# Kernel tuning notes

Hardware: AMD Instinct MI355X
Metric: run time of the kernel (lower is better)

The kernel has to match this reference:

```python
import jax, jax.numpy as jnp
import numpy as np

S = 15      # subject_nums
C = 2048    # in_channels (extractor output dim)
NC = 3      # num_classes
B = 1024    # subject_batch_num (rows per subject)
SUBJ = 7    # target subject
KERNEL_MUL = 2.0
KERNEL_NUM = 5


def setup_inputs() -> dict:
    key = jax.random.key(0)
    k = jax.random.split(key, 5)
    x = jax.random.normal(k[0], (S * B, C), dtype=jnp.float32)
    labels = jax.random.randint(k[1], (S * B,), 0, NC)
    y = jax.nn.one_hot(labels, NC, dtype=jnp.float32)
    subject_label = jnp.repeat(jnp.arange(S, dtype=jnp.int32), B)
    W_add = 0.02 * jax.random.normal(k[2], (S, 512, C), dtype=jnp.float32)
    b_add = jnp.zeros((S, 512), dtype=jnp.float32)
    W_cls = 0.02 * jax.random.normal(k[3], (S, NC, 512), dtype=jnp.float32)
    b_cls = jnp.zeros((S, NC), dtype=jnp.float32)
    return {"x": x, "y": y, "subject_label": subject_label,
            "W_add": W_add, "b_add": b_add, "W_cls": W_cls, "b_cls": b_cls,
            "subject": SUBJ}


def _mmd(source, target):
    # Standard multi-kernel Gaussian MMD (DAN-style), as used in the repo.
    n = source.shape[0]
    total = jnp.concatenate([source, target], axis=0)      # [2n, d]
    sq = jnp.sum(total * total, axis=-1)
    d2 = sq[:, None] + sq[None, :] - 2.0 * (total @ total.T)  # [2n, 2n]
    m = 2 * n
    bandwidth = jnp.sum(d2) / (m * m - m)
    bandwidth = bandwidth / (KERNEL_MUL ** (KERNEL_NUM // 2))
    kernels = sum(jnp.exp(-d2 / (bandwidth * (KERNEL_MUL ** i))) for i in range(KERNEL_NUM))
    XX = kernels[:n, :n]
    YY = kernels[n:, n:]
    XY = kernels[:n, n:]
    YX = kernels[n:, :n]
    return jnp.mean(XX + YY - XY - YX)


def reference(x, y, subject_label, W_add, b_add, W_cls, b_cls, subject):
    S_ = W_add.shape[0]
    b = x.shape[0] // S_          # == (subject_label == subject).sum() by construction
    K = S_ - 1
    idx = np.array([i for i in range(S_) if i != subject])  # static: subject is a Python int

    xr = x.reshape(S_, b, -1)
    src = xr[idx]                 # [K, b, C] source-subject blocks
    tgt = xr[subject]             # [b, C] target-subject block
    Wk, bk = W_add[idx], b_add[idx]

    # Grouped per-subject addblock Linear(C -> 512)
    outs = jnp.einsum('kbc,kdc->kbd', src, Wk) + bk[:, None, :]       # [K, b, 512]
    t_outs = jnp.einsum('bc,kdc->kbd', tgt, Wk) + bk[:, None, :]      # [K, b, 512]

    # Class predictors: ReLU + Linear(512 -> NC), predictors 0..K-1 are used
    Wc, bc = W_cls[:K], b_cls[:K]
    logits = jnp.einsum('kbd,knd->kbn', jax.nn.relu(outs), Wc) + bc[:, None, :]
    t_logits = jnp.einsum('kbd,knd->kbn', jax.nn.relu(t_outs), Wc) + bc[:, None, :]

    # ---- MMD loss ----
    mmd_loss = jnp.mean(jax.vmap(_mmd)(outs, t_outs))

    # ---- DISC loss: pairwise |softmax - softmax| over source features ----
    P = jax.nn.softmax(outs, axis=-1)                                  # [K, b, 512]
    disc_loss = 0.0
    for i in range(K - 1):  # fixed small loop over subjects, inner term vectorized
        disc_loss = disc_loss + jnp.abs(P[i + 1:] - P[i]).mean(axis=(1, 2)).sum()
    disc_loss = disc_loss * 2.0 / (K * (K - 1))

    # ---- CLS loss: KL(one-hot/soft target || log_softmax(logits)) ----
    yr = y.reshape(S_, b, -1)[idx]                                     # [K, b, NC]
    logp = jax.nn.log_softmax(logits, axis=-1)
    safe_y = jnp.where(yr > 0, yr, 1.0)
    kl = jnp.where(yr > 0, yr * (jnp.log(safe_y) - logp), 0.0)         # 0*log0 -> 0 (torch kl_div)
    cls_loss = kl.sum(-1).mean()

    # ---- PRED ACC on target subject ----
    t_prob = jax.nn.softmax(t_logits, axis=-1).mean(axis=0)            # [b, NC]
    y_tgt = y.reshape(S_, b, -1)[subject]
    pred = jnp.sum(jnp.argmax(t_prob, axis=1) == jnp.argmax(y_tgt, axis=1))
    nums = b

    return (mmd_loss * 0.1, disc_loss * 0.4, cls_loss, pred, nums)
```

## Files before the change

kernel.cpp:

```cpp
#include <hip/hip_runtime.h>
#include <hip/hip_bf16.h>
#include <stdint.h>

typedef __attribute__((ext_vector_type(8))) __bf16 bf16x8;
typedef __attribute__((ext_vector_type(4))) float f32x4;

#define CDIM 2048
#define DDIM 512

__device__ __forceinline__ unsigned short f2bf(float f) {
  union { float f; unsigned u; } a; a.f = f;
  unsigned r = a.u + 0x7FFFu + ((a.u >> 16) & 1u);
  return (unsigned short)(r >> 16);
}
__device__ __forceinline__ float bf2f(unsigned short h) {
  union { unsigned u; float f; } a; a.u = ((unsigned)h) << 16;
  return a.f;
}

typedef const __attribute__((address_space(1))) void gas_void;
typedef __attribute__((address_space(3))) void las_void;
__device__ __forceinline__ void async16(const void* g, void* l) {
  __builtin_amdgcn_global_load_lds((gas_void*)g, (las_void*)l, 16, 0, 0);
}

#define VMW(n) asm volatile("s_waitcnt vmcnt(" #n ")" ::: "memory")
#define SBAR() __builtin_amdgcn_s_barrier()
#define SFENCE() __builtin_amdgcn_sched_barrier(0)

__device__ __forceinline__ float blockSum256(float v) {
  __shared__ float sh[4];
  #pragma unroll
  for (int o = 32; o; o >>= 1) v += __shfl_xor(v, o, 64);
  int lane = threadIdx.x & 63, w = threadIdx.x >> 6;
  __syncthreads();
  if (lane == 0) sh[w] = v;
  __syncthreads();
  return sh[0] + sh[1] + sh[2] + sh[3];
}

__device__ __forceinline__ bf16x8 lds_frag(const unsigned short* base, int row, int cb) {
  return *(const bf16x8*)(base + row*64 + (((cb ^ (row & 7))) << 3));
}

__global__ __launch_bounds__(256) void k_convert(const float* __restrict__ x,
    const float* __restrict__ w, uint2* __restrict__ x16, uint2* __restrict__ w16) {
  const int nx4 = 15*1024*CDIM/4;
  const int nw4 = 15*DDIM*CDIM/4;
  int stride = gridDim.x * blockDim.x;
  for (int i = blockIdx.x*blockDim.x + threadIdx.x; i < nx4; i += stride) {
    float4 v = ((const float4*)x)[i];
    x16[i] = make_uint2((unsigned)f2bf(v.x) | ((unsigned)f2bf(v.y) << 16),
                        (unsigned)f2bf(v.z) | ((unsigned)f2bf(v.w) << 16));
  }
  for (int i = blockIdx.x*blockDim.x + threadIdx.x; i < nw4; i += stride) {
    float4 v = ((const float4*)w)[i];
    w16[i] = make_uint2((unsigned)f2bf(v.x) | ((unsigned)f2bf(v.y) << 16),
                        (unsigned)f2bf(v.z) | ((unsigned)f2bf(v.w) << 16));
  }
}

__global__ __launch_bounds__(512, 2) void k_gemm1(
    const unsigned short* __restrict__ x16,
    const unsigned short* __restrict__ w16,
    const float* __restrict__ b_add,
    const int* __restrict__ subj_p,
    unsigned short* __restrict__ t16)
{
  const int subj = *subj_p;
  int bid = blockIdx.x;
  int k  = bid >> 5;
  int t  = bid & 31;
  int mt = t >> 1, nt = t & 1;
  int ik = (k < subj) ? k : (k + 1);

  __shared__ unsigned short lds[3*384*64];

  int tid = threadIdx.x;
  int lane = tid & 63;
  int w = tid >> 6;
  int wm = w >> 2, wn = w & 3;
  int rr = lane >> 3;
  int cc8 = ((lane & 7) ^ rr) << 3;

  const unsigned short* Bb = w16 + (size_t)ik * DDIM * CDIM;

  f32x4 acc[4][4];
  #pragma unroll
  for (int a = 0; a < 4; a++)
    #pragma unroll
    for (int b = 0; b < 4; b++) acc[a][b] = f32x4{0.f,0.f,0.f,0.f};

  auto stage = [&](int tt, int bufi) {
    unsigned short* buf = lds + bufi*(384*64);
    int ks = tt*64;
    #pragma unroll
    for (int i = 0; i < 2; i++) {
      int r0 = (w*2 + i)*8;
      int gr = mt*128 + r0 + rr;
      int xrow = ((gr < 1024) ? ik : subj)*1024 + (gr & 1023);
      async16(x16 + (size_t)xrow*CDIM + ks + cc8, buf + r0*64);
    }
    #pragma unroll
    for (int i = 0; i < 4; i++) {
      int r0 = (w*4 + i)*8;
      int gn = nt*256 + r0 + rr;
      async16(Bb + (size_t)gn*CDIM + ks + cc8, buf + 8192 + r0*64);
    }
  };

  auto compute = [&](int bufi) {
    const unsigned short* A = lds + bufi*(384*64);
    const unsigned short* B = A + 8192;
    bf16x8 af[4][2], bfr[4][2];
    #pragma unroll
    for (int a = 0; a < 4; a++)
      #pragma unroll
      for (int ksl = 0; ksl < 2; ksl++)
        af[a][ksl] = lds_frag(A, wm*64 + a*16 + (lane & 15), ksl*4 + (lane >> 4));
    #pragma unroll
    for (int bb = 0; bb < 4; bb++)
      #pragma unroll
      for (int ksl = 0; ksl < 2; ksl++)
        bfr[bb][ksl] = lds_frag(B, wn*64 + bb*16 + (lane & 15), ksl*4 + (lane >> 4));
    __builtin_amdgcn_s_setprio(1);
    #pragma unroll
    for (int a = 0; a < 4; a++)
      #pragma unroll
      for (int bb = 0; bb < 4; bb++) {
        acc[a][bb] = __builtin_amdgcn_mfma_f32_16x16x32_bf16(af[a][0], bfr[bb][0], acc[a][bb], 0, 0, 0);
        acc[a][bb] = __builtin_amdgcn_mfma_f32_16x16x32_bf16(af[a][1], bfr[bb][1], acc[a][bb], 0, 0, 0);
      }
    __builtin_amdgcn_s_setprio(0);
  };

  stage(0, 0);
  stage(1, 1);
  VMW(6); SBAR(); SFENCE();

  int cur = 0;
  for (int tt = 0; tt < 30; ++tt) {
    int nb = cur + 2; if (nb >= 3) nb -= 3;
    stage(tt + 2, nb);
    compute(cur);
    VMW(6); SBAR(); SFENCE();
    cur = (cur == 2) ? 0 : cur + 1;
  }
  compute(cur);
  VMW(0); SBAR(); SFENCE();
  cur = (cur == 2) ? 0 : cur + 1;
  compute(cur);

  const float* bias = b_add + ik*DDIM;
  #pragma unroll
  for (int bb = 0; bb < 4; bb++) {
    int coln = nt*256 + wn*64 + bb*16 + (lane & 15);
    float bv = bias[coln];
    #pragma unroll
    for (int a = 0; a < 4; a++) {
      #pragma unroll
      for (int r = 0; r < 4; r++) {
        int rowm = mt*128 + wm*64 + a*16 + ((lane >> 4) << 2) + r;
        t16[((size_t)k*2048 + rowm)*DDIM + coln] = f2bf(acc[a][bb][r] + bv);
      }
    }
  }
}

__global__ __launch_bounds__(256) void k_rowred(const unsigned short* __restrict__ t16,
    float* __restrict__ sq, float* __restrict__ rmax, float* __restrict__ rinv)
{
  int wid = blockIdx.x*4 + (threadIdx.x >> 6);
  int lane = threadIdx.x & 63;
  uint4 v = *(const uint4*)(t16 + (size_t)wid * DDIM + lane*8);
  unsigned uu[4] = {v.x, v.y, v.z, v.w};
  float f[8];
  #pragma unroll
  for (int q = 0; q < 4; q++) {
    f[2*q]   = bf2f((unsigned short)(uu[q] & 0xffffu));
    f[2*q+1] = bf2f((unsigned short)(uu[q] >> 16));
  }
  float s2 = 0.f, mx = -3.4e38f;
  #pragma unroll
  for (int j = 0; j < 8; j++) { s2 += f[j]*f[j]; mx = fmaxf(mx, f[j]); }
  #pragma unroll
  for (int o = 32; o; o >>= 1) { s2 += __shfl_xor(s2, o, 64); mx = fmaxf(mx, __shfl_xor(mx, o, 64)); }
  float se = 0.f;
  #pragma unroll
  for (int j = 0; j < 8; j++) se += __expf(f[j] - mx);
  #pragma unroll
  for (int o = 32; o; o >>= 1) se += __shfl_xor(se, o, 64);
  if (lane == 0) { sq[wid] = s2; rmax[wid] = mx; rinv[wid] = 1.f/se; }
}

__global__ __launch_bounds__(256) void k_colsum(const unsigned short* __restrict__ t16,
    float* __restrict__ scol)
{
  int b = blockIdx.x;
  int k = b >> 4, sub = b & 15;
  int d = ((sub & 1) << 8) + threadIdx.x;
  int r0 = (sub >> 1) << 8;
  const unsigned short* base = t16 + (size_t)k*2048*DDIM;
  float s = 0.f;
  for (int r = r0; r < r0 + 256; r++) s += bf2f(base[(size_t)r*DDIM + d]);
  atomicAdd(&scol[k*DDIM + d], s);
}

__global__ __launch_bounds__(256) void k_bw(const float* __restrict__ sq,
    const float* __restrict__ scol, float* __restrict__ c2)
{
  int k = blockIdx.x;
  float a = 0.f;
  for (int r = threadIdx.x; r < 2048; r += 256) a += sq[k*2048 + r];
  float b = 0.f;
  for (int d = threadIdx.x; d < 512; d += 256) { float v = scol[k*512 + d]; b += v*v; }
  float atot = blockSum256(a);
  float btot = blockSum256(b);
  if (threadIdx.x == 0) {
    float sumd2 = 2.f*2048.f*atot - 2.f*btot;
    float bw = sumd2 / (2048.f*2048.f - 2048.f) * 0.25f;
    #pragma unroll
    for (int i = 0; i < 5; i++)
      c2[k*5 + i] = -1.4426950408889634f / (bw * (float)(1 << i));
  }
}

__global__ __launch_bounds__(256, 1) void k_mmd(
    const unsigned short* __restrict__ t16,
    const float* __restrict__ sq,
    const float* __restrict__ c2,
    float* __restrict__ g_acc)
{
  int bid = blockIdx.x;
  int k = bid / 136;
  int tri = bid - k*136;
  int it = 0;
  while (tri >= 16 - it) { tri -= 16 - it; it++; }
  int jt = it + tri;

  const unsigned short* T = t16 + (size_t)k * 2048 * DDIM;

  __shared__ unsigned short lds[3*256*64];
  __shared__ float sqs[256];

  int tid = threadIdx.x;
  int lane = tid & 63;
  int w = tid >> 6;
  int wm = w >> 1, wn = w & 1;
  int rr = lane >> 3;
  int cc8 = ((lane & 7) ^ rr) << 3;

  f32x4 acc[4][4];
  #pragma unroll
  for (int a = 0; a < 4; a++)
    #pragma unroll
    for (int b = 0; b < 4; b++) acc[a][b] = f32x4{0.f,0.f,0.f,0.f};

  auto stage = [&](int tt, int bufi) {
    unsigned short* buf = lds + bufi*(256*64);
    int ks = tt*64;
    #pragma unroll
    for (int i = 0; i < 4; i++) {
      int r0 = (w*4 + i)*8;
      async16(T + (size_t)(it*128 + r0 + rr)*DDIM + ks + cc8, buf + r0*64);
    }
    #pragma unroll
    for (int i = 0; i < 4; i++) {
      int r0 = (w*4 + i)*8;
      async16(T + (size_t)(jt*128 + r0 + rr)*DDIM + ks + cc8, buf + 8192 + r0*64);
    }
  };

  auto compute = [&](int bufi) {
    const unsigned short* A = lds + bufi*(256*64);
    const unsigned short* B = A + 8192;
    bf16x8 af[4][2], bfr[4][2];
    #pragma unroll
    for (int a = 0; a < 4; a++)
      #pragma unroll
      for (int ksl = 0; ksl < 2; ksl++)
        af[a][ksl] = lds_frag(A, wm*64 + a*16 + (lane & 15), ksl*4 + (lane >> 4));
    #pragma unroll
    for (int bb = 0; bb < 4; bb++)
      #pragma unroll
      for (int ksl = 0; ksl < 2; ksl++)
        bfr[bb][ksl] = lds_frag(B, wn*64 + bb*16 + (lane & 15), ksl*4 + (lane >> 4));
    __builtin_amdgcn_s_setprio(1);
    #pragma unroll
    for (int a = 0; a < 4; a++)
      #pragma unroll
      for (int bb = 0; bb < 4; bb++) {
        acc[a][bb] = __builtin_amdgcn_mfma_f32_16x16x32_bf16(af[a][0], bfr[bb][0], acc[a][bb], 0, 0, 0);
        acc[a][bb] = __builtin_amdgcn_mfma_f32_16x16x32_bf16(af[a][1], bfr[bb][1], acc[a][bb], 0, 0, 0);
      }
    __builtin_amdgcn_s_setprio(0);
  };

  stage(0, 0);
  stage(1, 1);
  VMW(8); SBAR(); SFENCE();

  int cur = 0;
  for (int tt = 0; tt < 6; ++tt) {
    int nb = cur + 2; if (nb >= 3) nb -= 3;
    stage(tt + 2, nb);
    compute(cur);
    VMW(8); SBAR(); SFENCE();
    cur = (cur == 2) ? 0 : cur + 1;
  }
  compute(cur);
  VMW(0); SBAR(); SFENCE();
  cur = (cur == 2) ? 0 : cur + 1;
  compute(cur);

  if (tid < 128) sqs[tid] = sq[k*2048 + it*128 + tid];
  else           sqs[tid] = sq[k*2048 + jt*128 + (tid - 128)];
  __syncthreads();

  float c0 = c2[k*5], c1 = c2[k*5+1], cA = c2[k*5+2], c3 = c2[k*5+3], c4 = c2[k*5+4];
  float part = 0.f;
  #pragma unroll
  for (int a = 0; a < 4; a++) {
    #pragma unroll
    for (int bb = 0; bb < 4; bb++) {
      int rj = wn*64 + bb*16 + (lane & 15);
      float sj = sqs[128 + rj];
      #pragma unroll
      for (int r = 0; r < 4; r++) {
        int ri = wm*64 + a*16 + ((lane >> 4) << 2) + r;
        float d2 = sqs[ri] + sj - 2.f*acc[a][bb][r];
        part += exp2f(c0*d2) + exp2f(c1*d2) + exp2f(cA*d2) + exp2f(c3*d2) + exp2f(c4*d2);
      }
    }
  }
  float tot = blockSum256(part);
  if (tid == 0) {
    float sgn = ((it < 8) == (jt < 8)) ? 1.f : -1.f;
    float wgt = (it == jt) ? 1.f : 2.f;
    atomicAdd(&g_acc[k], sgn * wgt * tot);
  }
}

__global__ __launch_bounds__(256) void k_heads(const unsigned short* __restrict__ t16,
    const float* __restrict__ rmax, const float* __restrict__ rinv,
    const float* __restrict__ W_cls, const float* __restrict__ b_cls,
    const float* __restrict__ y, const int* __restrict__ subj_p,
    float* __restrict__ g_acc, float* __restrict__ pacc)
{
  if (blockIdx.x < 2048) {
    int b = blockIdx.x;
    int row = b >> 1;
    int d = ((b & 1) << 8) + threadIdx.x;
    float p[14];
    #pragma unroll
    for (int k = 0; k < 14; k++) {
      float tv = bf2f(t16[((size_t)(k*2048 + row))*DDIM + d]);
      p[k] = __expf(tv - rmax[k*2048 + row]) * rinv[k*2048 + row];
    }
    float s = 0.f;
    #pragma unroll
    for (int i2 = 0; i2 < 14; i2++)
      #pragma unroll
      for (int j2 = i2+1; j2 < 14; j2++)
        s += fabsf(p[i2] - p[j2]);
    float tot = blockSum256(s);
    if (threadIdx.x == 0) atomicAdd(&g_acc[14 + (b & 7)], tot);
  } else {
    __shared__ float shk[4];
    int bid = blockIdx.x - 2048;
    int w = threadIdx.x >> 6;
    int lane = threadIdx.x & 63;
    int wid = bid*4 + w;
    int k = wid >> 11, r = wid & 2047;
    uint4 v = *(const uint4*)(t16 + (size_t)wid * DDIM + lane*8);
    unsigned uu[4] = {v.x, v.y, v.z, v.w};
    float f[8];
    #pragma unroll
    for (int q = 0; q < 4; q++) {
      f[2*q]   = fmaxf(bf2f((unsigned short)(uu[q] & 0xffffu)), 0.f);
      f[2*q+1] = fmaxf(bf2f((unsigned short)(uu[q] >> 16)), 0.f);
    }
    const float* Wc = W_cls + k*3*DDIM;
    int d0 = lane*8;
    float l0 = 0.f, l1 = 0.f, l2 = 0.f;
    #pragma unroll
    for (int j = 0; j < 8; j++) {
      l0 += f[j]*Wc[d0+j];
      l1 += f[j]*Wc[DDIM + d0+j];
      l2 += f[j]*Wc[2*DDIM + d0+j];
    }
    #pragma unroll
    for (int o = 32; o; o >>= 1) {
      l0 += __shfl_xor(l0, o, 64); l1 += __shfl_xor(l1, o, 64); l2 += __shfl_xor(l2, o, 64);
    }
    if (r < 1024) {
      if (lane == 0) {
        l0 += b_cls[k*3+0]; l1 += b_cls[k*3+1]; l2 += b_cls[k*3+2];
        float mx = fmaxf(l0, fmaxf(l1, l2));
        float lse = mx + __logf(__expf(l0-mx) + __expf(l1-mx) + __expf(l2-mx));
        int subj = *subj_p;
        int ik = (k < subj) ? k : k+1;
        const float* yr = y + ((size_t)(ik*1024 + r))*3;
        float tl = (yr[0] > 0.5f) ? l0 : ((yr[1] > 0.5f) ? l1 : l2);
        shk[w] = lse - tl;
      }
      __syncthreads();
      if (threadIdx.x == 0)
        atomicAdd(&g_acc[22 + k], shk[0] + shk[1] + shk[2] + shk[3]);
    } else {
      if (lane == 0) {
        l0 += b_cls[k*3+0]; l1 += b_cls[k*3+1]; l2 += b_cls[k*3+2];
        float mx = fmaxf(l0, fmaxf(l1, l2));
        float e0 = __expf(l0-mx), e1 = __expf(l1-mx), e2 = __expf(l2-mx);
        float inv = 1.f/(e0+e1+e2);
        int j = r - 1024;
        atomicAdd(&pacc[j*3 + 0], e0*inv);
        atomicAdd(&pacc[j*3 + 1], e1*inv);
        atomicAdd(&pacc[j*3 + 2], e2*inv);
      }
    }
  }
}

__global__ __launch_bounds__(256) void k_pred(const float* __restrict__ pacc,
    const float* __restrict__ y, const int* __restrict__ subj_p, float* __restrict__ g_acc)
{
  int j = blockIdx.x*256 + threadIdx.x;
  int subj = *subj_p;
  float p0 = pacc[j*3+0], p1 = pacc[j*3+1], p2 = pacc[j*3+2];
  int pa = 0; float pm = p0;
  if (p1 > pm) { pa = 1; pm = p1; }
  if (p2 > pm) { pa = 2; }
  const float* yt = y + ((size_t)(subj*1024 + j))*3;
  int ya = 0; float ym = yt[0];
  if (yt[1] > ym) { ya = 1; ym = yt[1]; }
  if (yt[2] > ym) { ya = 2; }
  float tot = blockSum256((pa == ya) ? 1.f : 0.f);
  if (threadIdx.x == 0) atomicAdd(&g_acc[36], tot);
}

__global__ void k_fin(const float* __restrict__ g_acc, float* __restrict__ out)
{
  if (threadIdx.x == 0 && blockIdx.x == 0) {
    float s = 0.f;
    for (int k = 0; k < 14; k++) s += g_acc[k];
    float disc = 0.f;
    for (int i = 14; i < 22; i++) disc += g_acc[i];
    float cls = 0.f;
    for (int i = 22; i < 36; i++) cls += g_acc[i];
    out[0] = 0.1f * s / (14.f * 1024.f * 1024.f);
    out[1] = 0.4f * disc * (2.f / (14.f*13.f)) / (1024.f*512.f);
    out[2] = cls / (14.f*1024.f);
    out[3] = g_acc[36];
    out[4] = 1024.f;
  }
}

extern "C" void kernel_launch(void* const* d_in, const int* in_sizes, int n_in,
                              void* d_out, int out_size, void* d_ws, size_t ws_size,
                              hipStream_t stream)
{
  (void)in_sizes; (void)n_in; (void)out_size; (void)ws_size;
  const float* x     = (const float*)d_in[0];
  const float* y     = (const float*)d_in[1];
  const float* W_add = (const float*)d_in[3];
  const float* b_add = (const float*)d_in[4];
  const float* W_cls = (const float*)d_in[5];
  const float* b_cls = (const float*)d_in[6];
  const int*   subj  = (const int*)d_in[7];

  char* ws = (char*)d_ws;
  size_t o = 0;
  auto take = [&](size_t b) { char* p = ws + o; o += (b + 255) & ~(size_t)255; return p; };
  unsigned short* X16 = (unsigned short*)take((size_t)15*1024*2048*2);
  unsigned short* W16 = (unsigned short*)take((size_t)15*512*2048*2);
  unsigned short* T16 = (unsigned short*)take((size_t)14*2048*512*2);
  float* SQ   = (float*)take((size_t)14*2048*4);
  float* RMAX = (float*)take((size_t)14*2048*4);
  float* RINV = (float*)take((size_t)14*2048*4);
  float* C2   = (float*)take(512);
  float* SCOL = (float*)take((size_t)14*512*4);
  float* PACC = (float*)take((size_t)1024*3*4);
  float* ACC  = (float*)take(256);

  hipMemsetAsync(SCOL, 0, 14*512*4 + 1024*3*4 + 256, stream);

  k_convert<<<2048, 256, 0, stream>>>(x, W_add, (uint2*)X16, (uint2*)W16);
  k_gemm1 <<<14*32, 512, 0, stream>>>(X16, W16, b_add, subj, T16);
  k_rowred<<<14*2048/4, 256, 0, stream>>>(T16, SQ, RMAX, RINV);
  k_colsum<<<14*16, 256, 0, stream>>>(T16, SCOL);
  k_bw    <<<14, 256, 0, stream>>>(SQ, SCOL, C2);
  k_mmd   <<<14*136, 256, 0, stream>>>(T16, SQ, C2, ACC);
  k_heads <<<2048 + 14*2048/4, 256, 0, stream>>>(T16, RMAX, RINV, W_cls, b_cls, y, subj, ACC, PACC);
  k_pred  <<<4, 256, 0, stream>>>(PACC, y, subj, ACC);
  k_fin   <<<1, 64, 0, stream>>>(ACC, (float*)d_out);
}
```

Before: 502.0 us.

## Fuse column sums into GEMM epilogue, square exps in MMD, remap blocks for L2

Column sums for the bandwidth are now accumulated in the first GEMM's epilogue with shuffles and atomics, which removes the separate k_colsum pass over T16. The five Gaussian kernels are computed from a single exp2 by repeated squaring, since their bandwidths are powers of two. The MMD kernel drops from triple to double buffering to fit two blocks per CU. Both GEMM grids are remapped so that blocks are interleaved across 8 subjects, likely to improve L2/XCD locality. Repeated squaring can lose a little accuracy, the column sums now use pre-rounding fp32 values, and double buffering exposes more load latency per block.

```diff
diff --git a/kernel.cpp b/kernel.cpp
--- a/kernel.cpp
+++ b/kernel.cpp
@@ -65,13 +65,15 @@
     const unsigned short* __restrict__ w16,
     const float* __restrict__ b_add,
     const int* __restrict__ subj_p,
-    unsigned short* __restrict__ t16)
-{
+    unsigned short* __restrict__ t16,
+    float* __restrict__ scol)
+{
+  int bid = blockIdx.x;
+  int k, t;
+  if (bid < 256) { k = bid & 7; t = bid >> 3; }
+  else { int b2 = bid - 256; k = 8 + (b2 & 7); t = b2 >> 3; if (k >= 14) return; }
+  int mt = t >> 1, nt = t & 1;
   const int subj = *subj_p;
-  int bid = blockIdx.x;
-  int k  = bid >> 5;
-  int t  = bid & 31;
-  int mt = t >> 1, nt = t & 1;
   int ik = (k < subj) ? k : (k + 1);
 
   __shared__ unsigned short lds[3*384*64];
@@ -156,14 +158,20 @@
   for (int bb = 0; bb < 4; bb++) {
     int coln = nt*256 + wn*64 + bb*16 + (lane & 15);
     float bv = bias[coln];
+    float cs = 0.f;
     #pragma unroll
     for (int a = 0; a < 4; a++) {
       #pragma unroll
       for (int r = 0; r < 4; r++) {
         int rowm = mt*128 + wm*64 + a*16 + ((lane >> 4) << 2) + r;
-        t16[((size_t)k*2048 + rowm)*DDIM + coln] = f2bf(acc[a][bb][r] + bv);
-      }
-    }
+        float val = acc[a][bb][r] + bv;
+        t16[((size_t)k*2048 + rowm)*DDIM + coln] = f2bf(val);
+        cs += val;
+      }
+    }
+    cs += __shfl_xor(cs, 16, 64);
+    cs += __shfl_xor(cs, 32, 64);
+    if ((lane >> 4) == 0) atomicAdd(&scol[k*DDIM + coln], cs);
   }
 }
 
@@ -191,19 +199,6 @@
   #pragma unroll
   for (int o = 32; o; o >>= 1) se += __shfl_xor(se, o, 64);
   if (lane == 0) { sq[wid] = s2; rmax[wid] = mx; rinv[wid] = 1.f/se; }
-}
-
-__global__ __launch_bounds__(256) void k_colsum(const unsigned short* __restrict__ t16,
-    float* __restrict__ scol)
-{
-  int b = blockIdx.x;
-  int k = b >> 4, sub = b & 15;
-  int d = ((sub & 1) << 8) + threadIdx.x;
-  int r0 = (sub >> 1) << 8;
-  const unsigned short* base = t16 + (size_t)k*2048*DDIM;
-  float s = 0.f;
-  for (int r = r0; r < r0 + 256; r++) s += bf2f(base[(size_t)r*DDIM + d]);
-  atomicAdd(&scol[k*DDIM + d], s);
 }
 
 __global__ __launch_bounds__(256) void k_bw(const float* __restrict__ sq,
@@ -225,22 +220,24 @@
   }
 }
 
-__global__ __launch_bounds__(256, 1) void k_mmd(
+__global__ __launch_bounds__(256, 2) void k_mmd(
     const unsigned short* __restrict__ t16,
     const float* __restrict__ sq,
     const float* __restrict__ c2,
     float* __restrict__ g_acc)
 {
   int bid = blockIdx.x;
-  int k = bid / 136;
-  int tri = bid - k*136;
+  int k, pr;
+  if (bid < 1088) { k = bid & 7; pr = bid >> 3; }
+  else { int b2 = bid - 1088; k = 8 + (b2 & 7); pr = b2 >> 3; if (k >= 14) return; }
+  int tri = pr;
   int it = 0;
   while (tri >= 16 - it) { tri -= 16 - it; it++; }
   int jt = it + tri;
 
   const unsigned short* T = t16 + (size_t)k * 2048 * DDIM;
 
-  __shared__ unsigned short lds[3*256*64];
+  __shared__ unsigned short lds[2*256*64];
   __shared__ float sqs[256];
 
   int tid = threadIdx.x;
@@ -297,27 +294,22 @@
   };
 
   stage(0, 0);
-  stage(1, 1);
-  VMW(8); SBAR(); SFENCE();
+  VMW(0); SBAR(); SFENCE();
 
   int cur = 0;
-  for (int tt = 0; tt < 6; ++tt) {
-    int nb = cur + 2; if (nb >= 3) nb -= 3;
-    stage(tt + 2, nb);
+  for (int tt = 0; tt < 7; ++tt) {
+    stage(tt + 1, cur ^ 1);
     compute(cur);
-    VMW(8); SBAR(); SFENCE();
-    cur = (cur == 2) ? 0 : cur + 1;
-  }
-  compute(cur);
-  VMW(0); SBAR(); SFENCE();
-  cur = (cur == 2) ? 0 : cur + 1;
+    VMW(0); SBAR(); SFENCE();
+    cur ^= 1;
+  }
   compute(cur);
 
   if (tid < 128) sqs[tid] = sq[k*2048 + it*128 + tid];
   else           sqs[tid] = sq[k*2048 + jt*128 + (tid - 128)];
   __syncthreads();
 
-  float c0 = c2[k*5], c1 = c2[k*5+1], cA = c2[k*5+2], c3 = c2[k*5+3], c4 = c2[k*5+4];
+  float c4 = c2[k*5 + 4];
   float part = 0.f;
   #pragma unroll
   for (int a = 0; a < 4; a++) {
@@ -329,7 +321,9 @@
       for (int r = 0; r < 4; r++) {
         int ri = wm*64 + a*16 + ((lane >> 4) << 2) + r;
         float d2 = sqs[ri] + sj - 2.f*acc[a][bb][r];
-        part += exp2f(c0*d2) + exp2f(c1*d2) + exp2f(cA*d2) + exp2f(c3*d2) + exp2f(c4*d2);
+        float z = exp2f(c4*d2);
+        float z2 = z*z, z4 = z2*z2, z8 = z4*z4;
+        part += z + z2 + z4 + z8 + z8*z8;
       }
     }
   }
@@ -486,11 +480,10 @@
   hipMemsetAsync(SCOL, 0, 14*512*4 + 1024*3*4 + 256, stream);
 
   k_convert<<<2048, 256, 0, stream>>>(x, W_add, (uint2*)X16, (uint2*)W16);
-  k_gemm1 <<<14*32, 512, 0, stream>>>(X16, W16, b_add, subj, T16);
+  k_gemm1 <<<512, 512, 0, stream>>>(X16, W16, b_add, subj, T16, SCOL);
   k_rowred<<<14*2048/4, 256, 0, stream>>>(T16, SQ, RMAX, RINV);
-  k_colsum<<<14*16, 256, 0, stream>>>(T16, SCOL);
   k_bw    <<<14, 256, 0, stream>>>(SQ, SCOL, C2);
-  k_mmd   <<<14*136, 256, 0, stream>>>(T16, SQ, C2, ACC);
+  k_mmd   <<<2176, 256, 0, stream>>>(T16, SQ, C2, ACC);
   k_heads <<<2048 + 14*2048/4, 256, 0, stream>>>(T16, RMAX, RINV, W_cls, b_cls, y, subj, ACC, PACC);
   k_pred  <<<4, 256, 0, stream>>>(PACC, y, subj, ACC);
   k_fin   <<<1, 64, 0, stream>>>(ACC, (float*)d_out);
```

Result: faster. 451.9 us (-10.0%).
